# Kernel tuning notes

Hardware: AMD Instinct MI355X
Metric: run time of the kernel (lower is better)

The kernel has to match this reference:

```python
import jax, jax.numpy as jnp
import numpy as np

WSCALE = 0.05  # keep qk logits in a stable range for softmax

def setup_inputs() -> dict:
    key = jax.random.key(0)
    ks = jax.random.split(key, 7)
    B, C, H, W = 8, 256, 64, 64
    d = C // 8
    x = jax.random.normal(ks[0], (B, C, H, W), dtype=jnp.float32)
    Wq = jax.random.normal(ks[1], (d, C), dtype=jnp.float32) * WSCALE
    Wk = jax.random.normal(ks[2], (d, C), dtype=jnp.float32) * WSCALE
    Wv = jax.random.normal(ks[3], (C, C), dtype=jnp.float32) * WSCALE
    bq = jnp.zeros((d,), jnp.float32)
    bk = jnp.zeros((d,), jnp.float32)
    bv = jnp.zeros((C,), jnp.float32)
    return {"x": x, "Wq": Wq, "bq": bq, "Wk": Wk, "bk": bk, "Wv": Wv, "bv": bv}

def reference(x, Wq, bq, Wk, bk, Wv, bv):
    B, C, H, W = x.shape
    N = H * W
    xf = x.reshape(B, C, N)                                  # [B,C,N]
    # 1x1 convs == per-pixel linear projections
    q = jnp.einsum('dc,bcn->bdn', Wq, xf) + bq[None, :, None]  # [B,d,N]
    k = jnp.einsum('dc,bcn->bdn', Wk, xf) + bk[None, :, None]  # [B,d,N]
    v = jnp.einsum('ec,bcn->ben', Wv, xf) + bv[None, :, None]  # [B,C,N]
    # attn[b,i,j] = q_i . k_j ; softmax over j (keys)
    attn = jax.nn.softmax(jnp.einsum('bdi,bdj->bij', q, k), axis=-1)  # [B,N,N]
    # out[b,c,i] = sum_j v[b,c,j] * attn[b,i,j]
    out = jnp.einsum('bcj,bij->bci', v, attn)                # [B,C,N]
    return out.reshape(B, C, H, W)
```

## Files before the change

kernel.cpp:

```cpp
#include <hip/hip_runtime.h>
#include <math.h>

#define NB 8
#define NC 256
#define ND 32
#define NN 4096
#define NM 320
#define LOG2E 1.44269504088896f
#define XSTR 264

typedef short short8 __attribute__((ext_vector_type(8)));
typedef short short4v __attribute__((ext_vector_type(4)));
typedef float f32x4 __attribute__((ext_vector_type(4)));

__device__ __forceinline__ unsigned int f2bf_u(float f) {
    return (__float_as_uint(f) + 0x8000u) >> 16;
}
__device__ __forceinline__ unsigned short f2bf(float f) {
    return (unsigned short)f2bf_u(f);
}

__global__ __launch_bounds__(256) void repack_kernel(
    const float* __restrict__ Wq, const float* __restrict__ bq,
    const float* __restrict__ Wk, const float* __restrict__ bk,
    const float* __restrict__ Wv, const float* __restrict__ bv,
    unsigned short* __restrict__ wp, float* __restrict__ bias)
{
    const int T    = blockIdx.x * 256 + threadIdx.x;
    const int j    = T & 7;
    const int lane = (T >> 3) & 63;
    const int ks   = (T >> 9) & 7;
    const int mt   = T >> 12;
    const int m = mt * 16 + (lane & 15);
    const int k = ks * 32 + ((lane >> 4) << 3) + j;
    float wv;
    if (m < 32)       wv = Wq[m * NC + k] * LOG2E;
    else if (m < 64)  wv = Wk[(m - 32) * NC + k];
    else              wv = Wv[(m - 64) * NC + k];
    wp[T] = f2bf(wv);
    if (T < NM) {
        float bb;
        if (T < 32)      bb = bq[T] * LOG2E;
        else if (T < 64) bb = bk[T - 32];
        else             bb = bv[T - 64];
        bias[T] = bb;
    }
}

__global__ __launch_bounds__(256, 4) void proj_kernel(
    const float* __restrict__ x,
    const unsigned short* __restrict__ wp,
    const float* __restrict__ bias,
    unsigned short* __restrict__ q_ws,
    unsigned short* __restrict__ k_ws,
    unsigned short* __restrict__ v_ws)
{
    __shared__ __align__(16) unsigned short xs[32 * XSTR];

    const int b  = blockIdx.x >> 7;
    const int n0 = (blockIdx.x & 127) << 5;
    const int t  = threadIdx.x;

    {
        const int n  = t & 31;
        const int cg = t >> 5;
        const float* xb = x + (size_t)b * NC * NN + n0 + n;
        #pragma unroll
        for (int it = 0; it < 8; ++it) {
            const int c = 32 * it + 4 * cg;
            const float x0 = xb[(size_t)(c + 0) * NN];
            const float x1 = xb[(size_t)(c + 1) * NN];
            const float x2 = xb[(size_t)(c + 2) * NN];
            const float x3 = xb[(size_t)(c + 3) * NN];
            uint2 pk;
            pk.x = (f2bf_u(x1) << 16) | f2bf_u(x0);
            pk.y = (f2bf_u(x3) << 16) | f2bf_u(x2);
            *(uint2*)(xs + n * XSTR + c) = pk;
        }
    }
    __syncthreads();

    const int w    = t >> 6;
    const int lane = t & 63;
    const int li = lane & 15;
    const int qd = lane >> 4;

    f32x4 acc[5][2];
    #pragma unroll
    for (int u = 0; u < 5; ++u) {
        const float bb = bias[(w + 4 * u) * 16 + li];
        acc[u][0] = (f32x4){bb, bb, bb, bb};
        acc[u][1] = (f32x4){bb, bb, bb, bb};
    }

    #pragma unroll
    for (int ks = 0; ks < 8; ++ks) {
        short8 af[2];
        #pragma unroll
        for (int mt = 0; mt < 2; ++mt)
            af[mt] = *(const short8*)(xs + (mt * 16 + li) * XSTR + ks * 32 + qd * 8);
        #pragma unroll
        for (int u = 0; u < 5; ++u) {
            const int ct = w + 4 * u;
            const short8 bf = *(const short8*)(wp + (size_t)((ct * 8 + ks) * 64 + lane) * 8);
            acc[u][0] = __builtin_amdgcn_mfma_f32_16x16x32_bf16(af[0], bf, acc[u][0], 0, 0, 0);
            acc[u][1] = __builtin_amdgcn_mfma_f32_16x16x32_bf16(af[1], bf, acc[u][1], 0, 0, 0);
        }
    }

    #pragma unroll
    for (int u = 0; u < 5; ++u) {
        const int ct = w + 4 * u;
        if (ct < 2) {
            const int d = ct * 16 + li;
            #pragma unroll
            for (int mt = 0; mt < 2; ++mt)
                #pragma unroll
                for (int r = 0; r < 4; ++r) {
                    const int n = n0 + mt * 16 + 4 * qd + r;
                    q_ws[((size_t)b * NN + n) * ND + d] = f2bf(acc[u][mt][r]);
                }
        } else if (ct < 4) {
            const int d = (ct & 1) * 16 + li;
            #pragma unroll
            for (int mt = 0; mt < 2; ++mt)
                #pragma unroll
                for (int r = 0; r < 4; ++r) {
                    const int n = n0 + mt * 16 + 4 * qd + r;
                    k_ws[((size_t)(b * 256 + (n >> 4)) * 64 + (d >> 3) * 16 + (n & 15)) * 8 + (d & 7)]
                        = f2bf(acc[u][mt][r]);
                }
        } else {
            const int ctv = ct - 4;
            #pragma unroll
            for (int mt = 0; mt < 2; ++mt) {
                const int jt = (n0 >> 4) + mt;
                uint2 pk;
                pk.x = (f2bf_u(acc[u][mt][1]) << 16) | f2bf_u(acc[u][mt][0]);
                pk.y = (f2bf_u(acc[u][mt][3]) << 16) | f2bf_u(acc[u][mt][2]);
                *(uint2*)(v_ws + (((size_t)(b * 16 + ctv) * 256 + jt) * 64 + qd * 16 + li) * 4) = pk;
            }
        }
    }
}

__global__ __launch_bounds__(256, 2) void attn_kernel(
    const unsigned short* __restrict__ q_ws,
    const unsigned short* __restrict__ k_ws,
    const unsigned short* __restrict__ v_ws,
    float* __restrict__ out)
{
    const int b  = blockIdx.x & 7;
    const int i0 = (blockIdx.x >> 3) * 64;
    const int w    = threadIdx.x >> 6;
    const int lane = threadIdx.x & 63;
    const int li = lane & 15;
    const int qd = lane >> 4;
    const int c0 = 64 * w;

    short8 qf[4];
    #pragma unroll
    for (int sb = 0; sb < 4; ++sb)
        qf[sb] = *(const short8*)(q_ws + ((size_t)b * NN + i0 + 16 * sb + li) * ND + qd * 8);

    const unsigned short* kfb = k_ws + ((size_t)b * 256 * 64 + lane) * 8;
    const unsigned short* vtb[4];
    #pragma unroll
    for (int ct = 0; ct < 4; ++ct)
        vtb[ct] = v_ws + (((size_t)(b * 16 + (c0 >> 4) + ct) * 256) * 64 + lane) * 4;

    f32x4 o[4][4];
    #pragma unroll
    for (int sb = 0; sb < 4; ++sb)
        #pragma unroll
        for (int ct = 0; ct < 4; ++ct)
            o[sb][ct] = (f32x4){0.f, 0.f, 0.f, 0.f};
    float l_loc[4] = {0.f, 0.f, 0.f, 0.f};
    const f32x4 z4 = {0.f, 0.f, 0.f, 0.f};

    short8 kHA[2], kHB[2];
    uint2  vs[4][2];
    uint2  pk[4][2];

    auto HALF = [&](int j0, short8 (&kc)[2], short8 (&kn)[2]) {
        const size_t f0 = (size_t)(j0 >> 4);
        kn[0] = *(const short8*)(kfb + (f0 + 2) * 512);
        kn[1] = *(const short8*)(kfb + (f0 + 3) * 512);
        vs[2][0] = *(const uint2*)(vtb[2] + (f0    ) * 256);
        vs[2][1] = *(const uint2*)(vtb[2] + (f0 + 1) * 256);
        vs[3][0] = *(const uint2*)(vtb[3] + (f0    ) * 256);
        vs[3][1] = *(const uint2*)(vtb[3] + (f0 + 1) * 256);
        #pragma unroll
        for (int sb = 0; sb < 4; ++sb)
            #pragma unroll
            for (int jt = 0; jt < 2; ++jt) {
                const f32x4 s = __builtin_amdgcn_mfma_f32_16x16x32_bf16(kc[jt], qf[sb], z4, 0, 0, 0);
                const float p0 = __builtin_amdgcn_exp2f(s[0]);
                const float p1 = __builtin_amdgcn_exp2f(s[1]);
                const float p2 = __builtin_amdgcn_exp2f(s[2]);
                const float p3 = __builtin_amdgcn_exp2f(s[3]);
                l_loc[sb] += (p0 + p1) + (p2 + p3);
                const unsigned u0 = __float_as_uint(p0) + 0x8000u;
                const unsigned u1 = __float_as_uint(p1) + 0x8000u;
                const unsigned u2 = __float_as_uint(p2) + 0x8000u;
                const unsigned u3 = __float_as_uint(p3) + 0x8000u;
                pk[sb][jt].x = __builtin_amdgcn_perm(u1, u0, 0x07060302u);
                pk[sb][jt].y = __builtin_amdgcn_perm(u3, u2, 0x07060302u);
            }
        #pragma unroll
        for (int sb = 0; sb < 4; ++sb)
            #pragma unroll
            for (int jt = 0; jt < 2; ++jt)
                o[sb][0] = __builtin_amdgcn_mfma_f32_16x16x16bf16_1k(
                    __builtin_bit_cast(short4v, vs[0][jt]),
                    __builtin_bit_cast(short4v, pk[sb][jt]), o[sb][0], 0, 0, 0);
        vs[0][0] = *(const uint2*)(vtb[0] + (f0 + 2) * 256);
        vs[0][1] = *(const uint2*)(vtb[0] + (f0 + 3) * 256);
        #pragma unroll
        for (int sb = 0; sb < 4; ++sb)
            #pragma unroll
            for (int jt = 0; jt < 2; ++jt)
                o[sb][1] = __builtin_amdgcn_mfma_f32_16x16x16bf16_1k(
                    __builtin_bit_cast(short4v, vs[1][jt]),
                    __builtin_bit_cast(short4v, pk[sb][jt]), o[sb][1], 0, 0, 0);
        vs[1][0] = *(const uint2*)(vtb[1] + (f0 + 2) * 256);
        vs[1][1] = *(const uint2*)(vtb[1] + (f0 + 3) * 256);
        #pragma unroll
        for (int sb = 0; sb < 4; ++sb)
            #pragma unroll
            for (int jt = 0; jt < 2; ++jt)
                o[sb][2] = __builtin_amdgcn_mfma_f32_16x16x16bf16_1k(
                    __builtin_bit_cast(short4v, vs[2][jt]),
                    __builtin_bit_cast(short4v, pk[sb][jt]), o[sb][2], 0, 0, 0);
        #pragma unroll
        for (int sb = 0; sb < 4; ++sb)
            #pragma unroll
            for (int jt = 0; jt < 2; ++jt)
                o[sb][3] = __builtin_amdgcn_mfma_f32_16x16x16bf16_1k(
                    __builtin_bit_cast(short4v, vs[3][jt]),
                    __builtin_bit_cast(short4v, pk[sb][jt]), o[sb][3], 0, 0, 0);
    };

    kHA[0] = *(const short8*)(kfb);
    kHA[1] = *(const short8*)(kfb + 512);
    vs[0][0] = *(const uint2*)(vtb[0]);
    vs[0][1] = *(const uint2*)(vtb[0] + 256);
    vs[1][0] = *(const uint2*)(vtb[1]);
    vs[1][1] = *(const uint2*)(vtb[1] + 256);

    #pragma unroll 1
    for (int t = 0; t < 64; ++t) {
        HALF(64 * t,      kHA, kHB);
        HALF(64 * t + 32, kHB, kHA);
    }

    #pragma unroll
    for (int sb = 0; sb < 4; ++sb) {
        l_loc[sb] += __shfl_xor(l_loc[sb], 16, 64);
        l_loc[sb] += __shfl_xor(l_loc[sb], 32, 64);
    }

    #pragma unroll
    for (int sb = 0; sb < 4; ++sb) {
        const float linv = 1.0f / l_loc[sb];
        #pragma unroll
        for (int ct = 0; ct < 4; ++ct) {
            const int c = c0 + ct * 16 + qd * 4;
            float* op = out + ((size_t)b * NC + c) * NN + i0 + 16 * sb + li;
            #pragma unroll
            for (int r = 0; r < 4; ++r)
                op[(size_t)r * NN] = o[sb][ct][r] * linv;
        }
    }
}

extern "C" void kernel_launch(void* const* d_in, const int* in_sizes, int n_in,
                              void* d_out, int out_size, void* d_ws, size_t ws_size,
                              hipStream_t stream) {
    const float* x  = (const float*)d_in[0];
    const float* Wq = (const float*)d_in[1];
    const float* bq = (const float*)d_in[2];
    const float* Wk = (const float*)d_in[3];
    const float* bk = (const float*)d_in[4];
    const float* Wv = (const float*)d_in[5];
    const float* bv = (const float*)d_in[6];
    float* out = (float*)d_out;

    unsigned short* q_ws = (unsigned short*)d_ws;
    unsigned short* k_ws = q_ws + (size_t)NB * NN * ND;
    unsigned short* v_ws = k_ws + (size_t)NB * NN * ND;
    unsigned short* wp   = v_ws + (size_t)NB * NC * NN;
    float*          bias = (float*)(wp + (size_t)NM * NC);

    repack_kernel<<<NM * NC / 256, 256, 0, stream>>>(Wq, bq, Wk, bk, Wv, bv, wp, bias);
    proj_kernel<<<NB * (NN / 32), 256, 0, stream>>>(x, wp, bias, q_ws, k_ws, v_ws);
    attn_kernel<<<NB * (NN / 64), 256, 0, stream>>>(q_ws, k_ws, v_ws, out);
}
```

Baseline: 227.4 us.

## Split attention wave work into 2 query halves x 2 channel halves

Each wave now handles 32 queries and 128 output channels instead of 64 queries and 64 channels. That halves the redundant QK^T MFMAs and exp2 work per wave, since each wave previously recomputed the full 64-query score tile. In exchange, each wave loads twice as many V fragments per key step and holds more V registers, which may raise register pressure and global load traffic.

Result: slower. 308.2 us (+35.6%).

```diff
diff --git a/kernel.cpp b/kernel.cpp
--- a/kernel.cpp
+++ b/kernel.cpp
@@ -156,42 +156,45 @@
     const int lane = threadIdx.x & 63;
     const int li = lane & 15;
     const int qd = lane >> 4;
-    const int c0 = 64 * w;
-
-    short8 qf[4];
-    #pragma unroll
-    for (int sb = 0; sb < 4; ++sb)
-        qf[sb] = *(const short8*)(q_ws + ((size_t)b * NN + i0 + 16 * sb + li) * ND + qd * 8);
+    const int sp = w & 1;
+    const int ch = w >> 1;
+    const int c0 = 128 * ch;
+
+    short8 qf[2];
+    #pragma unroll
+    for (int sb = 0; sb < 2; ++sb)
+        qf[sb] = *(const short8*)(q_ws + ((size_t)b * NN + i0 + 32 * sp + 16 * sb + li) * ND + qd * 8);
 
     const unsigned short* kfb = k_ws + ((size_t)b * 256 * 64 + lane) * 8;
-    const unsigned short* vtb[4];
-    #pragma unroll
-    for (int ct = 0; ct < 4; ++ct)
+    const unsigned short* vtb[8];
+    #pragma unroll
+    for (int ct = 0; ct < 8; ++ct)
         vtb[ct] = v_ws + (((size_t)(b * 16 + (c0 >> 4) + ct) * 256) * 64 + lane) * 4;
 
-    f32x4 o[4][4];
-    #pragma unroll
-    for (int sb = 0; sb < 4; ++sb)
-        #pragma unroll
-        for (int ct = 0; ct < 4; ++ct)
+    f32x4 o[2][8];
+    #pragma unroll
+    for (int sb = 0; sb < 2; ++sb)
+        #pragma unroll
+        for (int ct = 0; ct < 8; ++ct)
             o[sb][ct] = (f32x4){0.f, 0.f, 0.f, 0.f};
-    float l_loc[4] = {0.f, 0.f, 0.f, 0.f};
+    float l_loc[2] = {0.f, 0.f};
     const f32x4 z4 = {0.f, 0.f, 0.f, 0.f};
 
     short8 kHA[2], kHB[2];
-    uint2  vs[4][2];
-    uint2  pk[4][2];
+    uint2  vs[8][2];
+    uint2  pk[2][2];
 
     auto HALF = [&](int j0, short8 (&kc)[2], short8 (&kn)[2]) {
         const size_t f0 = (size_t)(j0 >> 4);
         kn[0] = *(const short8*)(kfb + (f0 + 2) * 512);
         kn[1] = *(const short8*)(kfb + (f0 + 3) * 512);
-        vs[2][0] = *(const uint2*)(vtb[2] + (f0    ) * 256);
-        vs[2][1] = *(const uint2*)(vtb[2] + (f0 + 1) * 256);
-        vs[3][0] = *(const uint2*)(vtb[3] + (f0    ) * 256);
-        vs[3][1] = *(const uint2*)(vtb[3] + (f0 + 1) * 256);
-        #pragma unroll
-        for (int sb = 0; sb < 4; ++sb)
+        #pragma unroll
+        for (int ct = 4; ct < 8; ++ct) {
+            vs[ct][0] = *(const uint2*)(vtb[ct] + (f0    ) * 256);
+            vs[ct][1] = *(const uint2*)(vtb[ct] + (f0 + 1) * 256);
+        }
+        #pragma unroll
+        for (int sb = 0; sb < 2; ++sb)
             #pragma unroll
             for (int jt = 0; jt < 2; ++jt) {
                 const f32x4 s = __builtin_amdgcn_mfma_f32_16x16x32_bf16(kc[jt], qf[sb], z4, 0, 0, 0);
@@ -208,45 +211,28 @@
                 pk[sb][jt].y = __builtin_amdgcn_perm(u3, u2, 0x07060302u);
             }
         #pragma unroll
-        for (int sb = 0; sb < 4; ++sb)
-            #pragma unroll
-            for (int jt = 0; jt < 2; ++jt)
-                o[sb][0] = __builtin_amdgcn_mfma_f32_16x16x16bf16_1k(
-                    __builtin_bit_cast(short4v, vs[0][jt]),
-                    __builtin_bit_cast(short4v, pk[sb][jt]), o[sb][0], 0, 0, 0);
-        vs[0][0] = *(const uint2*)(vtb[0] + (f0 + 2) * 256);
-        vs[0][1] = *(const uint2*)(vtb[0] + (f0 + 3) * 256);
-        #pragma unroll
-        for (int sb = 0; sb < 4; ++sb)
-            #pragma unroll
-            for (int jt = 0; jt < 2; ++jt)
-                o[sb][1] = __builtin_amdgcn_mfma_f32_16x16x16bf16_1k(
-                    __builtin_bit_cast(short4v, vs[1][jt]),
-                    __builtin_bit_cast(short4v, pk[sb][jt]), o[sb][1], 0, 0, 0);
-        vs[1][0] = *(const uint2*)(vtb[1] + (f0 + 2) * 256);
-        vs[1][1] = *(const uint2*)(vtb[1] + (f0 + 3) * 256);
-        #pragma unroll
-        for (int sb = 0; sb < 4; ++sb)
-            #pragma unroll
-            for (int jt = 0; jt < 2; ++jt)
-                o[sb][2] = __builtin_amdgcn_mfma_f32_16x16x16bf16_1k(
-                    __builtin_bit_cast(short4v, vs[2][jt]),
-                    __builtin_bit_cast(short4v, pk[sb][jt]), o[sb][2], 0, 0, 0);
-        #pragma unroll
-        for (int sb = 0; sb < 4; ++sb)
-            #pragma unroll
-            for (int jt = 0; jt < 2; ++jt)
-                o[sb][3] = __builtin_amdgcn_mfma_f32_16x16x16bf16_1k(
-                    __builtin_bit_cast(short4v, vs[3][jt]),
-                    __builtin_bit_cast(short4v, pk[sb][jt]), o[sb][3], 0, 0, 0);
+        for (int ct = 0; ct < 8; ++ct) {
+            #pragma unroll
+            for (int sb = 0; sb < 2; ++sb)
+                #pragma unroll
+                for (int jt = 0; jt < 2; ++jt)
+                    o[sb][ct] = __builtin_amdgcn_mfma_f32_16x16x16bf16_1k(
+                        __builtin_bit_cast(short4v, vs[ct][jt]),
+                        __builtin_bit_cast(short4v, pk[sb][jt]), o[sb][ct], 0, 0, 0);
+            if (ct < 4) {
+                vs[ct][0] = *(const uint2*)(vtb[ct] + (f0 + 2) * 256);
+                vs[ct][1] = *(const uint2*)(vtb[ct] + (f0 + 3) * 256);
+            }
+        }
     };
 
     kHA[0] = *(const short8*)(kfb);
     kHA[1] = *(const short8*)(kfb + 512);
-    vs[0][0] = *(const uint2*)(vtb[0]);
-    vs[0][1] = *(const uint2*)(vtb[0] + 256);
-    vs[1][0] = *(const uint2*)(vtb[1]);
-    vs[1][1] = *(const uint2*)(vtb[1] + 256);
+    #pragma unroll
+    for (int ct = 0; ct < 4; ++ct) {
+        vs[ct][0] = *(const uint2*)(vtb[ct]);
+        vs[ct][1] = *(const uint2*)(vtb[ct] + 256);
+    }
 
     #pragma unroll 1
     for (int t = 0; t < 64; ++t) {
@@ -255,18 +241,18 @@
     }
 
     #pragma unroll
-    for (int sb = 0; sb < 4; ++sb) {
+    for (int sb = 0; sb < 2; ++sb) {
         l_loc[sb] += __shfl_xor(l_loc[sb], 16, 64);
         l_loc[sb] += __shfl_xor(l_loc[sb], 32, 64);
     }
 
     #pragma unroll
-    for (int sb = 0; sb < 4; ++sb) {
+    for (int sb = 0; sb < 2; ++sb) {
         const float linv = 1.0f / l_loc[sb];
         #pragma unroll
-        for (int ct = 0; ct < 4; ++ct) {
+        for (int ct = 0; ct < 8; ++ct) {
             const int c = c0 + ct * 16 + qd * 4;
-            float* op = out + ((size_t)b * NC + c) * NN + i0 + 16 * sb + li;
+            float* op = out + ((size_t)b * NC + c) * NN + i0 + 32 * sp + 16 * sb + li;
             #pragma unroll
             for (int r = 0; r < 4; ++r)
                 op[(size_t)r * NN] = o[sb][ct][r] * linv;
```

## Software-pipeline QK score/exp of next key tile under current PV MFMAs

Applied to the files above, without the earlier changes.

Restructures the attention inner loop so the scores, exp2 and bf16 packing for the next 32-key tile are computed while the PV MFMAs for the current tile run. P fragments are double-buffered, the loop gets a prologue and epilogue, and V prefetch is spread evenly across the four channel groups. The aim is to hide exp/VALU latency behind matrix-core work, at the cost of more registers, which could lower occupancy or cause spills.

Measured after the change: 249.8 us. 1.1x slower.

```diff
diff --git a/kernel.cpp b/kernel.cpp
--- a/kernel.cpp
+++ b/kernel.cpp
@@ -178,81 +178,75 @@
     float l_loc[4] = {0.f, 0.f, 0.f, 0.f};
     const f32x4 z4 = {0.f, 0.f, 0.f, 0.f};
 
-    short8 kHA[2], kHB[2];
+    short8 kA[2], kB[2];
     uint2  vs[4][2];
-    uint2  pk[4][2];
-
-    auto HALF = [&](int j0, short8 (&kc)[2], short8 (&kn)[2]) {
-        const size_t f0 = (size_t)(j0 >> 4);
-        kn[0] = *(const short8*)(kfb + (f0 + 2) * 512);
-        kn[1] = *(const short8*)(kfb + (f0 + 3) * 512);
-        vs[2][0] = *(const uint2*)(vtb[2] + (f0    ) * 256);
-        vs[2][1] = *(const uint2*)(vtb[2] + (f0 + 1) * 256);
-        vs[3][0] = *(const uint2*)(vtb[3] + (f0    ) * 256);
-        vs[3][1] = *(const uint2*)(vtb[3] + (f0 + 1) * 256);
+    uint2  pkA[4][2], pkB[4][2];
+
+    auto SSTRIP = [&](int sb, short8 (&kS)[2], uint2 (&pkN)[4][2]) {
+        #pragma unroll
+        for (int jt = 0; jt < 2; ++jt) {
+            const f32x4 s = __builtin_amdgcn_mfma_f32_16x16x32_bf16(kS[jt], qf[sb], z4, 0, 0, 0);
+            const float p0 = __builtin_amdgcn_exp2f(s[0]);
+            const float p1 = __builtin_amdgcn_exp2f(s[1]);
+            const float p2 = __builtin_amdgcn_exp2f(s[2]);
+            const float p3 = __builtin_amdgcn_exp2f(s[3]);
+            l_loc[sb] += (p0 + p1) + (p2 + p3);
+            const unsigned u0 = __float_as_uint(p0) + 0x8000u;
+            const unsigned u1 = __float_as_uint(p1) + 0x8000u;
+            const unsigned u2 = __float_as_uint(p2) + 0x8000u;
+            const unsigned u3 = __float_as_uint(p3) + 0x8000u;
+            pkN[sb][jt].x = __builtin_amdgcn_perm(u1, u0, 0x07060302u);
+            pkN[sb][jt].y = __builtin_amdgcn_perm(u3, u2, 0x07060302u);
+        }
+    };
+
+    auto HALF = [&](size_t f0, short8 (&kS)[2], short8 (&kP)[2],
+                    uint2 (&pkC)[4][2], uint2 (&pkN)[4][2]) {
+        kP[0] = *(const short8*)(kfb + (f0 + 4) * 512);
+        kP[1] = *(const short8*)(kfb + (f0 + 5) * 512);
+        #pragma unroll
+        for (int g = 0; g < 4; ++g) {
+            #pragma unroll
+            for (int sb = 0; sb < 4; ++sb)
+                #pragma unroll
+                for (int jt = 0; jt < 2; ++jt)
+                    o[sb][g] = __builtin_amdgcn_mfma_f32_16x16x16bf16_1k(
+                        __builtin_bit_cast(short4v, vs[g][jt]),
+                        __builtin_bit_cast(short4v, pkC[sb][jt]), o[sb][g], 0, 0, 0);
+            vs[g][0] = *(const uint2*)(vtb[g] + (f0 + 2) * 256);
+            vs[g][1] = *(const uint2*)(vtb[g] + (f0 + 3) * 256);
+            SSTRIP(g, kS, pkN);
+        }
+    };
+
+    kA[0] = *(const short8*)(kfb);
+    kA[1] = *(const short8*)(kfb + 512);
+    #pragma unroll
+    for (int ct = 0; ct < 4; ++ct) {
+        vs[ct][0] = *(const uint2*)(vtb[ct]);
+        vs[ct][1] = *(const uint2*)(vtb[ct] + 256);
+    }
+    kB[0] = *(const short8*)(kfb + 2 * 512);
+    kB[1] = *(const short8*)(kfb + 3 * 512);
+    #pragma unroll
+    for (int sb = 0; sb < 4; ++sb)
+        SSTRIP(sb, kA, pkA);
+
+    #pragma unroll 1
+    for (int t = 0; t < 63; ++t) {
+        HALF((size_t)4 * t,     kB, kA, pkA, pkB);
+        HALF((size_t)4 * t + 2, kA, kB, pkB, pkA);
+    }
+    HALF((size_t)252, kB, kA, pkA, pkB);
+    #pragma unroll
+    for (int g = 0; g < 4; ++g)
         #pragma unroll
         for (int sb = 0; sb < 4; ++sb)
             #pragma unroll
-            for (int jt = 0; jt < 2; ++jt) {
-                const f32x4 s = __builtin_amdgcn_mfma_f32_16x16x32_bf16(kc[jt], qf[sb], z4, 0, 0, 0);
-                const float p0 = __builtin_amdgcn_exp2f(s[0]);
-                const float p1 = __builtin_amdgcn_exp2f(s[1]);
-                const float p2 = __builtin_amdgcn_exp2f(s[2]);
-                const float p3 = __builtin_amdgcn_exp2f(s[3]);
-                l_loc[sb] += (p0 + p1) + (p2 + p3);
-                const unsigned u0 = __float_as_uint(p0) + 0x8000u;
-                const unsigned u1 = __float_as_uint(p1) + 0x8000u;
-                const unsigned u2 = __float_as_uint(p2) + 0x8000u;
-                const unsigned u3 = __float_as_uint(p3) + 0x8000u;
-                pk[sb][jt].x = __builtin_amdgcn_perm(u1, u0, 0x07060302u);
-                pk[sb][jt].y = __builtin_amdgcn_perm(u3, u2, 0x07060302u);
-            }
-        #pragma unroll
-        for (int sb = 0; sb < 4; ++sb)
-            #pragma unroll
             for (int jt = 0; jt < 2; ++jt)
-                o[sb][0] = __builtin_amdgcn_mfma_f32_16x16x16bf16_1k(
-                    __builtin_bit_cast(short4v, vs[0][jt]),
-                    __builtin_bit_cast(short4v, pk[sb][jt]), o[sb][0], 0, 0, 0);
-        vs[0][0] = *(const uint2*)(vtb[0] + (f0 + 2) * 256);
-        vs[0][1] = *(const uint2*)(vtb[0] + (f0 + 3) * 256);
-        #pragma unroll
-        for (int sb = 0; sb < 4; ++sb)
-            #pragma unroll
-            for (int jt = 0; jt < 2; ++jt)
-                o[sb][1] = __builtin_amdgcn_mfma_f32_16x16x16bf16_1k(
-                    __builtin_bit_cast(short4v, vs[1][jt]),
-                    __builtin_bit_cast(short4v, pk[sb][jt]), o[sb][1], 0, 0, 0);
-        vs[1][0] = *(const uint2*)(vtb[1] + (f0 + 2) * 256);
-        vs[1][1] = *(const uint2*)(vtb[1] + (f0 + 3) * 256);
-        #pragma unroll
-        for (int sb = 0; sb < 4; ++sb)
-            #pragma unroll
-            for (int jt = 0; jt < 2; ++jt)
-                o[sb][2] = __builtin_amdgcn_mfma_f32_16x16x16bf16_1k(
-                    __builtin_bit_cast(short4v, vs[2][jt]),
-                    __builtin_bit_cast(short4v, pk[sb][jt]), o[sb][2], 0, 0, 0);
-        #pragma unroll
-        for (int sb = 0; sb < 4; ++sb)
-            #pragma unroll
-            for (int jt = 0; jt < 2; ++jt)
-                o[sb][3] = __builtin_amdgcn_mfma_f32_16x16x16bf16_1k(
-                    __builtin_bit_cast(short4v, vs[3][jt]),
-                    __builtin_bit_cast(short4v, pk[sb][jt]), o[sb][3], 0, 0, 0);
-    };
-
-    kHA[0] = *(const short8*)(kfb);
-    kHA[1] = *(const short8*)(kfb + 512);
-    vs[0][0] = *(const uint2*)(vtb[0]);
-    vs[0][1] = *(const uint2*)(vtb[0] + 256);
-    vs[1][0] = *(const uint2*)(vtb[1]);
-    vs[1][1] = *(const uint2*)(vtb[1] + 256);
-
-    #pragma unroll 1
-    for (int t = 0; t < 64; ++t) {
-        HALF(64 * t,      kHA, kHB);
-        HALF(64 * t + 32, kHB, kHA);
-    }
+                o[sb][g] = __builtin_amdgcn_mfma_f32_16x16x16bf16_1k(
+                    __builtin_bit_cast(short4v, vs[g][jt]),
+                    __builtin_bit_cast(short4v, pkB[sb][jt]), o[sb][g], 0, 0, 0);
 
     #pragma unroll
     for (int sb = 0; sb < 4; ++sb) {
```
